# Performance work log

Hardware: AMD Instinct MI355X
Metric: run time of the kernel (lower is better)

The kernel has to match this reference:

```python
import math
import jax, jax.numpy as jnp
import numpy as np

NUM_HEADS = 16
NUM_LANDMARKS = 64


def setup_inputs() -> dict:
    key = jax.random.key(0)
    ks = jax.random.split(key, 14)
    B, S, H, M = 2, 4096, 1024, 512
    p = 0.02
    return {
        "hidden_states": jax.random.normal(ks[0], (B, S, H), jnp.float32),
        "Wq": jax.random.normal(ks[1], (H, H), jnp.float32) * p,
        "bq": jnp.zeros((H,), jnp.float32),
        "Wk": jax.random.normal(ks[2], (H, H), jnp.float32) * p,
        "bk": jnp.zeros((H,), jnp.float32),
        "Wv": jax.random.normal(ks[3], (H, H), jnp.float32) * p,
        "bv": jnp.zeros((H,), jnp.float32),
        "Wo": jax.random.normal(ks[4], (H, H), jnp.float32) * p,
        "bo": jnp.zeros((H,), jnp.float32),
        "mem_keys": jax.random.normal(ks[5], (M, H), jnp.float32) * p,
        "mem_values": jax.random.normal(ks[6], (M, H), jnp.float32) * p,
        "gate_w": jax.random.normal(ks[7], (H, 1), jnp.float32) * p,
        "gate_b": jnp.zeros((1,), jnp.float32),
        "top_k": 32,
    }


def reference(hidden_states, Wq, bq, Wk, bk, Wv, bv, Wo, bo,
              mem_keys, mem_values, gate_w, gate_b, top_k):
    B, S, H = hidden_states.shape
    nh, L = NUM_HEADS, NUM_LANDMARKS
    hd = H // nh

    # ---- landmark selection ('attention' method, no external attn weights) ----
    importance = jnp.linalg.norm(hidden_states, axis=-1)           # [B,S]
    _, lm_idx = jax.lax.top_k(importance, L)                       # [B,L]
    lm_idx = jnp.sort(lm_idx, axis=-1)
    landmark_hidden = jnp.take_along_axis(
        hidden_states, lm_idx[..., None], axis=1)                  # [B,L,H]

    # ---- landmark attention: all tokens attend to L landmarks ----
    q = (hidden_states @ Wq + bq).reshape(B, S, nh, hd)
    k = (landmark_hidden @ Wk + bk).reshape(B, L, nh, hd)
    v = (landmark_hidden @ Wv + bv).reshape(B, L, nh, hd)
    scores = jnp.einsum('bshd,blhd->bhsl', q, k) / math.sqrt(hd)   # [B,nh,S,L]
    attn = jax.nn.softmax(scores, axis=-1)
    ctx = jnp.einsum('bhsl,blhd->bshd', attn, v).reshape(B, S, H)
    landmark_out = ctx @ Wo + bo                                   # [B,S,H]

    # ---- memory bank read (top-k over M memory slots) ----
    mscores = jnp.einsum('bsh,mh->bsm', hidden_states, mem_keys) / math.sqrt(H)
    top_scores, top_idx = jax.lax.top_k(mscores, top_k)            # [B,S,K]
    top_vals = mem_values[top_idx]                                 # [B,S,K,H]
    mattn = jax.nn.softmax(top_scores, axis=-1)
    mem_out = jnp.einsum('bsk,bskh->bsh', mattn, top_vals)         # [B,S,H]
    gate = jax.nn.sigmoid(hidden_states @ gate_w + gate_b)         # [B,S,1]
    mem_out = gate * mem_out

    return landmark_out + mem_out
```

## Files before the change

kernel.cpp:

```cpp
#include <hip/hip_runtime.h>
#include <math.h>

#define HDIM 1024
#define NHEAD 16
#define HD 64
#define LM 64
#define MS 512
#define KSEL 32
#define NB 2
#define NS 4096
#define NTOK (NB*NS)

typedef __attribute__((ext_vector_type(8))) short short8;
typedef __attribute__((ext_vector_type(4))) float f32x4;
typedef __attribute__((ext_vector_type(4))) unsigned short us4;

__device__ __forceinline__ unsigned short f2bf(float f) {
  unsigned int u = __float_as_uint(f);
  unsigned int r = (u + 0x7fffu + ((u >> 16) & 1u)) >> 16;
  return (unsigned short)r;
}
__device__ __forceinline__ float bf2f(unsigned short u) {
  return __uint_as_float(((unsigned int)u) << 16);
}

__device__ __forceinline__ void gload_lds16(const unsigned short* g, unsigned short* l) {
  __builtin_amdgcn_global_load_lds(
      (const __attribute__((address_space(1))) unsigned int*)g,
      (__attribute__((address_space(3))) unsigned int*)l,
      16, 0, 0);
}

__global__ __launch_bounds__(256) void imp_gate_kernel(
    const float* __restrict__ hs, const float* __restrict__ gw,
    const float* __restrict__ gb, float* __restrict__ imp,
    float* __restrict__ gate, unsigned short* __restrict__ hsb) {
  const int lane = threadIdx.x & 63, wave = threadIdx.x >> 6;
  const int row = blockIdx.x*4 + wave;
  float ss = 0.f, dg = 0.f;
#pragma unroll
  for (int c = 0; c < 4; ++c) {
    const int d = c*256 + lane*4;
    const float4 hv = *(const float4*)(hs + (size_t)row*HDIM + d);
    const float4 gv = *(const float4*)(gw + d);
    ss += hv.x*hv.x + hv.y*hv.y + hv.z*hv.z + hv.w*hv.w;
    dg += hv.x*gv.x + hv.y*gv.y + hv.z*gv.z + hv.w*gv.w;
    us4 hb;
    hb.x = f2bf(hv.x); hb.y = f2bf(hv.y); hb.z = f2bf(hv.z); hb.w = f2bf(hv.w);
    *(us4*)(hsb + (size_t)row*HDIM + d) = hb;
  }
#pragma unroll
  for (int off = 32; off > 0; off >>= 1) {
    ss += __shfl_xor(ss, off);
    dg += __shfl_xor(dg, off);
  }
  if (lane == 0) {
    imp[row] = ss;
    gate[row] = 1.f/(1.f + expf(-(dg + gb[0])));
  }
}

__global__ __launch_bounds__(256) void lm_count_kernel(
    const float* __restrict__ imp, int* __restrict__ cnt) {
  const int b = blockIdx.z;
  const int jc = blockIdx.y;
  const int i = blockIdx.x*256 + threadIdx.x;
  const float* v = imp + b*NS;
  const float mine = v[i];
  __shared__ float tile[1024];
  const int j0 = jc*1024;
  *(float4*)&tile[threadIdx.x*4] = *(const float4*)&v[j0 + threadIdx.x*4];
  __syncthreads();
  int c = 0;
#pragma unroll 8
  for (int p = 0; p < 1024; p += 4) {
    const float4 t = *(const float4*)&tile[p];
    c += (t.x > mine) || (t.x == mine && (j0+p+0) < i);
    c += (t.y > mine) || (t.y == mine && (j0+p+1) < i);
    c += (t.z > mine) || (t.z == mine && (j0+p+2) < i);
    c += (t.w > mine) || (t.w == mine && (j0+p+3) < i);
  }
  atomicAdd(&cnt[b*NS + i], c);
}

__global__ __launch_bounds__(256) void lm_sel_kernel(
    const int* __restrict__ cnt, int* __restrict__ lm_idx) {
  const int b = blockIdx.y;
  const int i = blockIdx.x*256 + threadIdx.x;
  const int c = cnt[b*NS + i];
  if (c < LM) lm_idx[b*LM + c] = i;
}

__global__ __launch_bounds__(256) void lm_gather_kernel(
    const unsigned short* __restrict__ hsb, const int* __restrict__ lmi,
    unsigned short* __restrict__ g) {
  const int j = blockIdx.x;
  const int b = j >> 6;
  const int idx = lmi[j];
  const us4 v = *(const us4*)(hsb + ((size_t)(b*NS + idx))*HDIM + threadIdx.x*4);
  *(us4*)(g + (size_t)j*HDIM + threadIdx.x*4) = v;
}

__global__ __launch_bounds__(256) void kvproj_gemm_kernel(
    const unsigned short* __restrict__ g, const unsigned short* __restrict__ Wkvt,
    float* __restrict__ part) {
  __shared__ __align__(16) unsigned short As[128*32];
  __shared__ __align__(16) unsigned short Bs[128*32];
  const int tid = threadIdx.x;
  const int lane = tid & 63, wave = tid >> 6;
  const int wr = wave >> 1, wc = wave & 1;
  const int col0 = blockIdx.x << 7;
  const int sp = blockIdx.y;
  const int k00 = sp << 8;

  f32x4 acc[4][4];
#pragma unroll
  for (int m = 0; m < 4; ++m)
#pragma unroll
    for (int n = 0; n < 4; ++n) acc[m][n] = (f32x4)(0.f);

  const int srow = tid >> 2;
  const int sk   = (tid & 3) << 3;
  const unsigned short* gA = g    + (size_t)srow*HDIM + sk;
  const unsigned short* gB = Wkvt + (size_t)(col0 + srow)*HDIM + sk;
  const int fr = lane & 15;
  const int fk = (lane >> 4) << 3;
  const int fg = lane >> 4;

  for (int k0 = k00; k0 < k00 + 256; k0 += 32) {
    gload_lds16(gA + k0,             As + tid*8);
    gload_lds16(gA + 64*HDIM + k0,   As + 2048 + tid*8);
    gload_lds16(gB + k0,             Bs + tid*8);
    gload_lds16(gB + 64*HDIM + k0,   Bs + 2048 + tid*8);
    __syncthreads();
    short8 af[4], bf[4];
#pragma unroll
    for (int m = 0; m < 4; ++m)
      af[m] = *(const short8*)&As[(wr*64 + m*16 + fr)*32 + fk];
#pragma unroll
    for (int n = 0; n < 4; ++n)
      bf[n] = *(const short8*)&Bs[(wc*64 + n*16 + fr)*32 + fk];
#pragma unroll
    for (int m = 0; m < 4; ++m)
#pragma unroll
      for (int n = 0; n < 4; ++n)
        acc[m][n] = __builtin_amdgcn_mfma_f32_16x16x32_bf16(af[m], bf[n], acc[m][n], 0, 0, 0);
    __syncthreads();
  }
#pragma unroll
  for (int m = 0; m < 4; ++m)
#pragma unroll
    for (int n = 0; n < 4; ++n) {
      const int colg = col0 + wc*64 + n*16 + fr;
#pragma unroll
      for (int r = 0; r < 4; ++r) {
        const int row = wr*64 + m*16 + fg*4 + r;
        part[((size_t)(sp*128 + row))*2048 + colg] = acc[m][n][r];
      }
    }
}

__global__ __launch_bounds__(256) void kv_reduce2_kernel(
    const float* __restrict__ part, const float* __restrict__ bk,
    const float* __restrict__ bv, float* __restrict__ kbuf,
    float* __restrict__ vbuf) {
  const int row = blockIdx.y;
  const int col = blockIdx.x*256 + threadIdx.x;
  float s = 0.f;
#pragma unroll
  for (int sp = 0; sp < 4; ++sp)
    s += part[((size_t)(sp*128 + row))*2048 + col];
  if (col < HDIM) kbuf[(size_t)row*HDIM + col] = s + bk[col];
  else            vbuf[(size_t)row*HDIM + col - HDIM] = s + bv[col - HDIM];
}

__global__ __launch_bounds__(256) void prep_kernel(
    const float* __restrict__ Wk, const float* __restrict__ Wv,
    const float* __restrict__ Wq, const float* __restrict__ Wo,
    const float* __restrict__ mk, const float* __restrict__ mv,
    unsigned short* __restrict__ Wkvt, unsigned short* __restrict__ Wcat,
    unsigned short* __restrict__ Wot, unsigned short* __restrict__ mvT) {
  const int z = blockIdx.z;
  __shared__ float tile[32][33];
  const int tx = threadIdx.x & 31, ty = threadIdx.x >> 5;
  if (z < 4) {
    const float* W = (z == 0) ? Wk : (z == 1) ? Wv : (z == 2) ? Wq : Wo;
    unsigned short* Wt = (z == 0) ? Wkvt
                       : (z == 1) ? (Wkvt + (size_t)HDIM*HDIM)
                       : (z == 2) ? Wcat : Wot;
    const int bx = blockIdx.x * 32, by = blockIdx.y * 32;
#pragma unroll
    for (int i = 0; i < 32; i += 8)
      tile[ty + i][tx] = W[(size_t)(by + ty + i)*HDIM + bx + tx];
    __syncthreads();
#pragma unroll
    for (int i = 0; i < 32; i += 8)
      Wt[(size_t)(bx + ty + i)*HDIM + by + tx] = f2bf(tile[tx][ty + i]);
  } else {
    const int blk = blockIdx.y*32 + blockIdx.x;
    if (blk < 512) {
      const int off = (blk << 10) + threadIdx.x*4;
      const float4 v = *(const float4*)&mk[off];
      us4 w;
      w.x = f2bf(v.x); w.y = f2bf(v.y); w.z = f2bf(v.z); w.w = f2bf(v.w);
      *(us4*)&(Wcat + (size_t)HDIM*HDIM)[off] = w;
    } else {
      const int t = blk - 512;
      const int by = (t >> 5) * 32;
      const int bx = (t & 31) * 32;
#pragma unroll
      for (int i = 0; i < 32; i += 8)
        tile[ty + i][tx] = mv[(size_t)(by + ty + i)*HDIM + bx + tx];
      __syncthreads();
#pragma unroll
      for (int i = 0; i < 32; i += 8)
        mvT[(size_t)(bx + ty + i)*MS + by + tx] = f2bf(tile[tx][ty + i]);
    }
  }
}

__global__ __launch_bounds__(256) void gemm_qmsc_kernel(
    const unsigned short* __restrict__ A, const unsigned short* __restrict__ Bt,
    const float* __restrict__ bq, unsigned short* __restrict__ qb,
    float* __restrict__ msc) {
  __shared__ __align__(16) unsigned short As[128*32];
  __shared__ __align__(16) unsigned short Bs[128*32];
  const int tid = threadIdx.x;
  const int lane = tid & 63, wave = tid >> 6;
  const int wr = wave >> 1, wc = wave & 1;
  const int wg = blockIdx.x;
  const int swz = (wg & 7)*96 + (wg >> 3);
  const int bx = swz % 12, by = swz / 12;
  const int row0 = by << 7, col0 = bx << 7;

  f32x4 acc[4][4];
#pragma unroll
  for (int m = 0; m < 4; ++m)
#pragma unroll
    for (int n = 0; n < 4; ++n) acc[m][n] = (f32x4)(0.f);

  const int srow = tid >> 2;
  const int sk   = (tid & 3) << 3;
  const unsigned short* gA = A  + (size_t)(row0 + srow)*HDIM + sk;
  const unsigned short* gB = Bt + (size_t)(col0 + srow)*HDIM + sk;
  const int fr = lane & 15;
  const int fk = (lane >> 4) << 3;
  const int fg = lane >> 4;

  for (int k0 = 0; k0 < HDIM; k0 += 32) {
    gload_lds16(gA + k0,             As + tid*8);
    gload_lds16(gA + 64*HDIM + k0,   As + 2048 + tid*8);
    gload_lds16(gB + k0,             Bs + tid*8);
    gload_lds16(gB + 64*HDIM + k0,   Bs + 2048 + tid*8);
    __syncthreads();
    short8 af[4], bf[4];
#pragma unroll
    for (int m = 0; m < 4; ++m)
      af[m] = *(const short8*)&As[(wr*64 + m*16 + fr)*32 + fk];
#pragma unroll
    for (int n = 0; n < 4; ++n)
      bf[n] = *(const short8*)&Bs[(wc*64 + n*16 + fr)*32 + fk];
#pragma unroll
    for (int m = 0; m < 4; ++m)
#pragma unroll
      for (int n = 0; n < 4; ++n)
        acc[m][n] = __builtin_amdgcn_mfma_f32_16x16x32_bf16(af[m], bf[n], acc[m][n], 0, 0, 0);
    __syncthreads();
  }

#pragma unroll
  for (int m = 0; m < 4; ++m) {
#pragma unroll
    for (int n = 0; n < 4; ++n) {
      const int col = col0 + wc*64 + n*16 + fr;
      if (col < HDIM) {
        const float bb = bq[col];
#pragma unroll
        for (int r = 0; r < 4; ++r) {
          const int row = row0 + wr*64 + m*16 + fg*4 + r;
          qb[(size_t)row*HDIM + col] = f2bf(acc[m][n][r] + bb);
        }
      } else {
        const int c2 = col - HDIM;
#pragma unroll
        for (int r = 0; r < 4; ++r) {
          const int row = row0 + wr*64 + m*16 + fg*4 + r;
          msc[(size_t)row*MS + c2] = acc[m][n][r]*0.03125f;
        }
      }
    }
  }
}

__global__ __launch_bounds__(256) void attn_mfma_kernel(
    const unsigned short* __restrict__ qb, const float* __restrict__ kbuf,
    const float* __restrict__ vbuf, unsigned short* __restrict__ ctxb) {
  const int tb = blockIdx.x, h = blockIdx.y, b = blockIdx.z;
  const int tid = threadIdx.x;
  const int lane = tid & 63, wave = tid >> 6;
  __shared__ __align__(16) unsigned short Qs[128*64];
  __shared__ __align__(16) unsigned short Ks[64*64];
  __shared__ __align__(16) unsigned short Vt[64*64];
  __shared__ __align__(16) unsigned short Ps[128*64];

  const int tok0 = b*NS + tb*128;
#pragma unroll
  for (int it = 0; it < 4; ++it) {
    const int idx = it*256 + tid;
    gload_lds16(qb + (size_t)(tok0 + (idx >> 3))*HDIM + h*64 + (idx & 7)*8,
                Qs + idx*8);
  }
#pragma unroll
  for (int it = 0; it < 4; ++it) {
    const int i = it*256 + tid;
    const int l = i >> 4, d0 = (i & 15) << 2;
    const size_t base = (size_t)(b*LM + l)*HDIM + h*64 + d0;
    const float4 kv = *(const float4*)(kbuf + base);
    const float4 vv = *(const float4*)(vbuf + base);
    us4 k4; k4.x = f2bf(kv.x); k4.y = f2bf(kv.y); k4.z = f2bf(kv.z); k4.w = f2bf(kv.w);
    *(us4*)&Ks[l*64 + d0] = k4;
    Vt[(d0+0)*64 + l] = f2bf(vv.x);
    Vt[(d0+1)*64 + l] = f2bf(vv.y);
    Vt[(d0+2)*64 + l] = f2bf(vv.z);
    Vt[(d0+3)*64 + l] = f2bf(vv.w);
  }
  __syncthreads();

  const int fr = lane & 15;
  const int fg = lane >> 4;
  const int fk = fg << 3;
  const int wrow = wave*32;

  f32x4 acc[2][4];
#pragma unroll
  for (int m = 0; m < 2; ++m)
#pragma unroll
    for (int n = 0; n < 4; ++n) acc[m][n] = (f32x4)(0.f);
#pragma unroll
  for (int ks = 0; ks < 2; ++ks) {
    short8 af[2], bf[4];
#pragma unroll
    for (int m = 0; m < 2; ++m)
      af[m] = *(const short8*)&Qs[(wrow + m*16 + fr)*64 + ks*32 + fk];
#pragma unroll
    for (int n = 0; n < 4; ++n)
      bf[n] = *(const short8*)&Ks[(n*16 + fr)*64 + ks*32 + fk];
#pragma unroll
    for (int m = 0; m < 2; ++m)
#pragma unroll
      for (int n = 0; n < 4; ++n)
        acc[m][n] = __builtin_amdgcn_mfma_f32_16x16x32_bf16(af[m], bf[n], acc[m][n], 0, 0, 0);
  }

#pragma unroll
  for (int m = 0; m < 2; ++m) {
#pragma unroll
    for (int r = 0; r < 4; ++r) {
      float p0 = acc[m][0][r]*0.125f, p1 = acc[m][1][r]*0.125f;
      float p2 = acc[m][2][r]*0.125f, p3 = acc[m][3][r]*0.125f;
      float mx = fmaxf(fmaxf(p0, p1), fmaxf(p2, p3));
#pragma unroll
      for (int off = 1; off < 16; off <<= 1) mx = fmaxf(mx, __shfl_xor(mx, off));
      p0 = expf(p0 - mx); p1 = expf(p1 - mx); p2 = expf(p2 - mx); p3 = expf(p3 - mx);
      float sm = p0 + p1 + p2 + p3;
#pragma unroll
      for (int off = 1; off < 16; off <<= 1) sm += __shfl_xor(sm, off);
      const float inv = 1.f/sm;
      const int prow = (wrow + m*16 + fg*4 + r)*64;
      Ps[prow + 0*16 + fr] = f2bf(p0*inv);
      Ps[prow + 1*16 + fr] = f2bf(p1*inv);
      Ps[prow + 2*16 + fr] = f2bf(p2*inv);
      Ps[prow + 3*16 + fr] = f2bf(p3*inv);
    }
  }
  __syncthreads();

  f32x4 occ[2][4];
#pragma unroll
  for (int m = 0; m < 2; ++m)
#pragma unroll
    for (int n = 0; n < 4; ++n) occ[m][n] = (f32x4)(0.f);
#pragma unroll
  for (int ks = 0; ks < 2; ++ks) {
    short8 af[2], bf[4];
#pragma unroll
    for (int m = 0; m < 2; ++m)
      af[m] = *(const short8*)&Ps[(wrow + m*16 + fr)*64 + ks*32 + fk];
#pragma unroll
    for (int n = 0; n < 4; ++n)
      bf[n] = *(const short8*)&Vt[(n*16 + fr)*64 + ks*32 + fk];
#pragma unroll
    for (int m = 0; m < 2; ++m)
#pragma unroll
      for (int n = 0; n < 4; ++n)
        occ[m][n] = __builtin_amdgcn_mfma_f32_16x16x32_bf16(af[m], bf[n], occ[m][n], 0, 0, 0);
  }
#pragma unroll
  for (int m = 0; m < 2; ++m)
#pragma unroll
    for (int n = 0; n < 4; ++n)
#pragma unroll
      for (int r = 0; r < 4; ++r)
        ctxb[(size_t)(tok0 + wrow + m*16 + fg*4 + r)*HDIM + h*64 + n*16 + fr] =
            f2bf(occ[m][n][r]);
}

__global__ __launch_bounds__(256) void sel_kernel(
    const float* __restrict__ msc, const float* __restrict__ gate,
    unsigned short* __restrict__ Wm) {
  const int tid = threadIdx.x;
  const int lane = tid & 63, wave = tid >> 6;
  const int token = blockIdx.x*4 + wave;

  __shared__ __align__(16) int s_hist[4][256];
  __shared__ unsigned long long s_list[4][256];
  __shared__ int s_B[4], s_above[4], s_nlist[4];

  *(int4*)&s_hist[wave][lane*4] = make_int4(0, 0, 0, 0);
  if (lane == 0) s_nlist[wave] = 0;

  float v[8];
#pragma unroll
  for (int j = 0; j < 8; ++j) v[j] = msc[(size_t)token*MS + j*64 + lane];

  float mx = v[0], mn = v[0];
#pragma unroll
  for (int j = 1; j < 8; ++j) { mx = fmaxf(mx, v[j]); mn = fminf(mn, v[j]); }
#pragma unroll
  for (int off = 32; off > 0; off >>= 1) {
    mx = fmaxf(mx, __shfl_xor(mx, off));
    mn = fminf(mn, __shfl_xor(mn, off));
  }
  const float range = mx - mn;
  const float scale = (range > 1e-20f) ? 255.f/range : 0.f;

  __builtin_amdgcn_wave_barrier();
  int bins[8];
#pragma unroll
  for (int j = 0; j < 8; ++j) {
    int b = (int)((v[j] - mn)*scale);
    bins[j] = b > 255 ? 255 : b;
    atomicAdd(&s_hist[wave][bins[j]], 1);
  }
  __builtin_amdgcn_wave_barrier();

  const int4 c = *(const int4*)&s_hist[wave][lane*4];
  const int lane_total = c.x + c.y + c.z + c.w;
  int sfx = lane_total;
#pragma unroll
  for (int off = 1; off < 64; off <<= 1) {
    const int src = lane + off;
    int y = __shfl(sfx, src < 64 ? src : lane);
    sfx += (src < 64) ? y : 0;
  }
  const int beyond = sfx - lane_total;
  const int s3 = c.w + beyond;
  const int s2 = c.z + s3;
  const int s1 = c.y + s2;
  const int s0 = c.x + s1;
  int Bl = -1, abv = 0;
  if (s0 >= KSEL && s1 < KSEL) { Bl = lane*4 + 0; abv = s1; }
  if (s1 >= KSEL && s2 < KSEL) { Bl = lane*4 + 1; abv = s2; }
  if (s2 >= KSEL && s3 < KSEL) { Bl = lane*4 + 2; abv = s3; }
  if (s3 >= KSEL && beyond < KSEL) { Bl = lane*4 + 3; abv = beyond; }
  if (Bl >= 0) { s_B[wave] = Bl; s_above[wave] = abv; }
  __builtin_amdgcn_wave_barrier();
  const int B = s_B[wave];
  const int rem = KSEL - s_above[wave];

#pragma unroll
  for (int j = 0; j < 8; ++j) {
    if (bins[j] == B) {
      const unsigned int u = __float_as_uint(v[j]);
      const unsigned int vk = (u & 0x80000000u) ? ~u : (u | 0x80000000u);
      const int p = atomicAdd(&s_nlist[wave], 1);
      if (p < 256)
        s_list[wave][p] = ((unsigned long long)vk << 32) | (unsigned int)~(j*64 + lane);
    }
  }
  __builtin_amdgcn_wave_barrier();

  const int nl = s_nlist[wave] < 256 ? s_nlist[wave] : 256;
  unsigned long long T = ~0ull;
  for (int r = 0; r < rem; ++r) {
    unsigned long long best = 0; int pos = -1;
    for (int i = lane; i < nl; i += 64)
      if (s_list[wave][i] > best) { best = s_list[wave][i]; pos = i; }
#pragma unroll
    for (int off = 32; off > 0; off >>= 1) {
      const unsigned long long ob = __shfl_xor(best, off);
      const int op = __shfl_xor(pos, off);
      if (ob > best) { best = ob; pos = op; }
    }
    if (lane == 0) s_list[wave][pos] = 0;
    T = best;
    __builtin_amdgcn_wave_barrier();
  }

  float e[8];
  float esum = 0.f;
#pragma unroll
  for (int j = 0; j < 8; ++j) {
    bool sel = bins[j] > B;
    if (!sel && bins[j] == B) {
      const unsigned int u = __float_as_uint(v[j]);
      const unsigned int vk = (u & 0x80000000u) ? ~u : (u | 0x80000000u);
      const unsigned long long key =
          ((unsigned long long)vk << 32) | (unsigned int)~(j*64 + lane);
      sel = key >= T;
    }
    e[j] = sel ? expf(v[j] - mx) : 0.f;
    esum += e[j];
  }
#pragma unroll
  for (int off = 32; off > 0; off >>= 1) esum += __shfl_xor(esum, off);
  const float ginv = gate[token]/esum;
#pragma unroll
  for (int j = 0; j < 8; ++j)
    Wm[(size_t)token*MS + j*64 + lane] = f2bf(e[j]*ginv);
}

__global__ __launch_bounds__(256) void gemm_fused_out_kernel(
    const unsigned short* __restrict__ A,
    const unsigned short* __restrict__ Bt,
    const unsigned short* __restrict__ Wm,
    const unsigned short* __restrict__ mvT,
    const float* __restrict__ bias, float* __restrict__ out) {
  __shared__ __align__(16) unsigned short As[128*32];
  __shared__ __align__(16) unsigned short Bs[128*32];
  const int tid = threadIdx.x;
  const int lane = tid & 63, wave = tid >> 6;
  const int wr = wave >> 1, wc = wave & 1;
  const int wg = blockIdx.x;
  const int swz = (wg & 7)*64 + (wg >> 3);
  const int bx = swz & 7, by = swz >> 3;
  const int row0 = by << 7, col0 = bx << 7;

  f32x4 acc[4][4];
#pragma unroll
  for (int m = 0; m < 4; ++m)
#pragma unroll
    for (int n = 0; n < 4; ++n) acc[m][n] = (f32x4)(0.f);

  const int srow = tid >> 2;
  const int sk   = (tid & 3) << 3;
  const int fr = lane & 15;
  const int fk = (lane >> 4) << 3;
  const int fg = lane >> 4;

  {
    const unsigned short* gA = A  + (size_t)(row0 + srow)*HDIM + sk;
    const unsigned short* gB = Bt + (size_t)(col0 + srow)*HDIM + sk;
    for (int k0 = 0; k0 < HDIM; k0 += 32) {
      gload_lds16(gA + k0,             As + tid*8);
      gload_lds16(gA + 64*HDIM + k0,   As + 2048 + tid*8);
      gload_lds16(gB + k0,             Bs + tid*8);
      gload_lds16(gB + 64*HDIM + k0,   Bs + 2048 + tid*8);
      __syncthreads();
      short8 af[4], bf[4];
#pragma unroll
      for (int m = 0; m < 4; ++m)
        af[m] = *(const short8*)&As[(wr*64 + m*16 + fr)*32 + fk];
#pragma unroll
      for (int n = 0; n < 4; ++n)
        bf[n] = *(const short8*)&Bs[(wc*64 + n*16 + fr)*32 + fk];
#pragma unroll
      for (int m = 0; m < 4; ++m)
#pragma unroll
        for (int n = 0; n < 4; ++n)
          acc[m][n] = __builtin_amdgcn_mfma_f32_16x16x32_bf16(af[m], bf[n], acc[m][n], 0, 0, 0);
      __syncthreads();
    }
  }
  {
    const unsigned short* gA = Wm  + (size_t)(row0 + srow)*MS + sk;
    const unsigned short* gB = mvT + (size_t)(col0 + srow)*MS + sk;
    for (int k0 = 0; k0 < MS; k0 += 32) {
      gload_lds16(gA + k0,           As + tid*8);
      gload_lds16(gA + 64*MS + k0,   As + 2048 + tid*8);
      gload_lds16(gB + k0,           Bs + tid*8);
      gload_lds16(gB + 64*MS + k0,   Bs + 2048 + tid*8);
      __syncthreads();
      short8 af[4], bf[4];
#pragma unroll
      for (int m = 0; m < 4; ++m)
        af[m] = *(const short8*)&As[(wr*64 + m*16 + fr)*32 + fk];
#pragma unroll
      for (int n = 0; n < 4; ++n)
        bf[n] = *(const short8*)&Bs[(wc*64 + n*16 + fr)*32 + fk];
#pragma unroll
      for (int m = 0; m < 4; ++m)
#pragma unroll
        for (int n = 0; n < 4; ++n)
          acc[m][n] = __builtin_amdgcn_mfma_f32_16x16x32_bf16(af[m], bf[n], acc[m][n], 0, 0, 0);
      __syncthreads();
    }
  }

#pragma unroll
  for (int m = 0; m < 4; ++m) {
#pragma unroll
    for (int n = 0; n < 4; ++n) {
      const int col = col0 + wc*64 + n*16 + fr;
      const float bb = bias[col];
#pragma unroll
      for (int r = 0; r < 4; ++r) {
        const int row = row0 + wr*64 + m*16 + fg*4 + r;
        out[(size_t)row*HDIM + col] = acc[m][n][r] + bb;
      }
    }
  }
}

extern "C" void kernel_launch(void* const* d_in, const int* in_sizes, int n_in,
                              void* d_out, int out_size, void* d_ws, size_t ws_size,
                              hipStream_t stream) {
  const float* hs = (const float*)d_in[0];
  const float* Wq = (const float*)d_in[1];
  const float* bq = (const float*)d_in[2];
  const float* Wk = (const float*)d_in[3];
  const float* bk = (const float*)d_in[4];
  const float* Wv = (const float*)d_in[5];
  const float* bv = (const float*)d_in[6];
  const float* Wo = (const float*)d_in[7];
  const float* bo = (const float*)d_in[8];
  const float* mk = (const float*)d_in[9];
  const float* mv = (const float*)d_in[10];
  const float* gw = (const float*)d_in[11];
  const float* gb = (const float*)d_in[12];
  float* out = (float*)d_out;

  char* ws = (char*)d_ws;
  unsigned short* hsb  = (unsigned short*)(ws);
  unsigned short* ctxb = hsb;
  unsigned short* qb   = (unsigned short*)(ws + ((size_t)16 << 20));
  unsigned short* Wm   = qb;
  float*          msc  = (float*)(ws + ((size_t)32 << 20));
  unsigned short* Wkvt = (unsigned short*)(ws + ((size_t)48 << 20));
  unsigned short* Wcat = (unsigned short*)(ws + ((size_t)52 << 20));
  unsigned short* Wot  = (unsigned short*)(ws + ((size_t)55 << 20));
  unsigned short* mvT  = (unsigned short*)(ws + ((size_t)57 << 20));
  float*          kbuf = (float*)(ws + ((size_t)58 << 20));
  float*          vbuf = (float*)(ws + ((size_t)58 << 20) + ((size_t)512 << 10));
  unsigned short* g    = (unsigned short*)(ws + ((size_t)59 << 20));
  float*          part = (float*)(ws + ((size_t)59 << 20) + ((size_t)256 << 10));
  float*          imp  = (float*)(ws + ((size_t)64 << 20));
  float*          gate = (float*)(ws + ((size_t)64 << 20) + ((size_t)32 << 10));
  int*            cnt  = (int*)  (ws + ((size_t)64 << 20) + ((size_t)64 << 10));
  int*            lmi  = (int*)  (ws + ((size_t)64 << 20) + ((size_t)96 << 10));

  imp_gate_kernel<<<dim3(NTOK/4), 256, 0, stream>>>(hs, gw, gb, imp, gate, hsb);
  hipMemsetAsync(cnt, 0, NB*NS*sizeof(int), stream);
  lm_count_kernel<<<dim3(NS/256, 4, NB), 256, 0, stream>>>(imp, cnt);
  lm_sel_kernel<<<dim3(NS/256, NB), 256, 0, stream>>>(cnt, lmi);
  prep_kernel<<<dim3(32, 32, 5), 256, 0, stream>>>(
      Wk, Wv, Wq, Wo, mk, mv, Wkvt, Wcat, Wot, mvT);
  lm_gather_kernel<<<dim3(NB*LM), 256, 0, stream>>>(hsb, lmi, g);
  kvproj_gemm_kernel<<<dim3(16, 4), 256, 0, stream>>>(g, Wkvt, part);
  kv_reduce2_kernel<<<dim3(8, 128), 256, 0, stream>>>(part, bk, bv, kbuf, vbuf);
  gemm_qmsc_kernel<<<dim3(768), 256, 0, stream>>>(hsb, Wcat, bq, qb, msc);
  attn_mfma_kernel<<<dim3(NS/128, NHEAD, NB), 256, 0, stream>>>(qb, kbuf, vbuf, ctxb);
  sel_kernel<<<dim3(NTOK/4), 256, 0, stream>>>(msc, gate, Wm);
  gemm_fused_out_kernel<<<dim3(512), 256, 0, stream>>>(ctxb, Wot, Wm, mvT, bo, out);
}
```

Before: 167.9 us.

## Use 64-wide XOR-swizzled K tiles in GEMMs and reuse Q LDS for P

Both bf16 MFMA GEMM kernels now stage 64-wide K slices per iteration instead of 32. Each thread loads four 16-byte chunks, and chunk positions are XOR-swizzled by row so the short8 fragment reads avoid LDS bank conflicts. This halves the number of barrier pairs per GEMM and doubles LDS use per block, which may lower occupancy. In the attention kernel the softmax probabilities are written into the Q shared buffer instead of a separate P buffer, and the barrier before the PV product is dropped. That relies on each wave reading back only its own rows.

Result: faster. 163.6 us (-2.5%).

```diff
diff --git a/kernel.cpp b/kernel.cpp
--- a/kernel.cpp
+++ b/kernel.cpp
@@ -30,6 +30,15 @@
       (__attribute__((address_space(3))) unsigned int*)l,
       16, 0, 0);
 }
+
+#define STAGE64(gbase, k0, LDA, lds)                                          \
+  {                                                                           \
+    const unsigned short* _s = (gbase) + (k0) + gchk*8;                       \
+    gload_lds16(_s,                 (lds) + tid*8);                           \
+    gload_lds16(_s + (size_t)32*(LDA), (lds) + 2048 + tid*8);                 \
+    gload_lds16(_s + (size_t)64*(LDA), (lds) + 4096 + tid*8);                 \
+    gload_lds16(_s + (size_t)96*(LDA), (lds) + 6144 + tid*8);                 \
+  }
 
 __global__ __launch_bounds__(256) void imp_gate_kernel(
     const float* __restrict__ hs, const float* __restrict__ gw,
@@ -223,8 +232,8 @@
     const unsigned short* __restrict__ A, const unsigned short* __restrict__ Bt,
     const float* __restrict__ bq, unsigned short* __restrict__ qb,
     float* __restrict__ msc) {
-  __shared__ __align__(16) unsigned short As[128*32];
-  __shared__ __align__(16) unsigned short Bs[128*32];
+  __shared__ __align__(16) unsigned short As[128*64];
+  __shared__ __align__(16) unsigned short Bs[128*64];
   const int tid = threadIdx.x;
   const int lane = tid & 63, wave = tid >> 6;
   const int wr = wave >> 1, wc = wave & 1;
@@ -239,32 +248,35 @@
 #pragma unroll
     for (int n = 0; n < 4; ++n) acc[m][n] = (f32x4)(0.f);
 
-  const int srow = tid >> 2;
-  const int sk   = (tid & 3) << 3;
-  const unsigned short* gA = A  + (size_t)(row0 + srow)*HDIM + sk;
-  const unsigned short* gB = Bt + (size_t)(col0 + srow)*HDIM + sk;
+  const int srow = tid >> 3;
+  const int gchk = (tid & 7) ^ (srow & 7);
+  const unsigned short* gA = A  + (size_t)(row0 + srow)*HDIM;
+  const unsigned short* gB = Bt + (size_t)(col0 + srow)*HDIM;
   const int fr = lane & 15;
-  const int fk = (lane >> 4) << 3;
   const int fg = lane >> 4;
-
-  for (int k0 = 0; k0 < HDIM; k0 += 32) {
-    gload_lds16(gA + k0,             As + tid*8);
-    gload_lds16(gA + 64*HDIM + k0,   As + 2048 + tid*8);
-    gload_lds16(gB + k0,             Bs + tid*8);
-    gload_lds16(gB + 64*HDIM + k0,   Bs + 2048 + tid*8);
+  const int ca = ((0*4 + fg) ^ (fr & 7)) * 8;
+  const int cb = ((1*4 + fg) ^ (fr & 7)) * 8;
+
+  for (int k0 = 0; k0 < HDIM; k0 += 64) {
+    STAGE64(gA, k0, HDIM, As);
+    STAGE64(gB, k0, HDIM, Bs);
     __syncthreads();
-    short8 af[4], bf[4];
-#pragma unroll
-    for (int m = 0; m < 4; ++m)
-      af[m] = *(const short8*)&As[(wr*64 + m*16 + fr)*32 + fk];
-#pragma unroll
-    for (int n = 0; n < 4; ++n)
-      bf[n] = *(const short8*)&Bs[(wc*64 + n*16 + fr)*32 + fk];
-#pragma unroll
-    for (int m = 0; m < 4; ++m)
+#pragma unroll
+    for (int kh = 0; kh < 2; ++kh) {
+      const int cc = kh ? cb : ca;
+      short8 af[4], bf[4];
+#pragma unroll
+      for (int m = 0; m < 4; ++m)
+        af[m] = *(const short8*)&As[(wr*64 + m*16 + fr)*64 + cc];
 #pragma unroll
       for (int n = 0; n < 4; ++n)
-        acc[m][n] = __builtin_amdgcn_mfma_f32_16x16x32_bf16(af[m], bf[n], acc[m][n], 0, 0, 0);
+        bf[n] = *(const short8*)&Bs[(wc*64 + n*16 + fr)*64 + cc];
+#pragma unroll
+      for (int m = 0; m < 4; ++m)
+#pragma unroll
+        for (int n = 0; n < 4; ++n)
+          acc[m][n] = __builtin_amdgcn_mfma_f32_16x16x32_bf16(af[m], bf[n], acc[m][n], 0, 0, 0);
+    }
     __syncthreads();
   }
 
@@ -301,7 +313,6 @@
   __shared__ __align__(16) unsigned short Qs[128*64];
   __shared__ __align__(16) unsigned short Ks[64*64];
   __shared__ __align__(16) unsigned short Vt[64*64];
-  __shared__ __align__(16) unsigned short Ps[128*64];
 
   const int tok0 = b*NS + tb*128;
 #pragma unroll
@@ -367,13 +378,12 @@
       for (int off = 1; off < 16; off <<= 1) sm += __shfl_xor(sm, off);
       const float inv = 1.f/sm;
       const int prow = (wrow + m*16 + fg*4 + r)*64;
-      Ps[prow + 0*16 + fr] = f2bf(p0*inv);
-      Ps[prow + 1*16 + fr] = f2bf(p1*inv);
-      Ps[prow + 2*16 + fr] = f2bf(p2*inv);
-      Ps[prow + 3*16 + fr] = f2bf(p3*inv);
-    }
-  }
-  __syncthreads();
+      Qs[prow + 0*16 + fr] = f2bf(p0*inv);
+      Qs[prow + 1*16 + fr] = f2bf(p1*inv);
+      Qs[prow + 2*16 + fr] = f2bf(p2*inv);
+      Qs[prow + 3*16 + fr] = f2bf(p3*inv);
+    }
+  }
 
   f32x4 occ[2][4];
 #pragma unroll
@@ -385,7 +395,7 @@
     short8 af[2], bf[4];
 #pragma unroll
     for (int m = 0; m < 2; ++m)
-      af[m] = *(const short8*)&Ps[(wrow + m*16 + fr)*64 + ks*32 + fk];
+      af[m] = *(const short8*)&Qs[(wrow + m*16 + fr)*64 + ks*32 + fk];
 #pragma unroll
     for (int n = 0; n < 4; ++n)
       bf[n] = *(const short8*)&Vt[(n*16 + fr)*64 + ks*32 + fk];
@@ -526,8 +536,8 @@
     const unsigned short* __restrict__ Wm,
     const unsigned short* __restrict__ mvT,
     const float* __restrict__ bias, float* __restrict__ out) {
-  __shared__ __align__(16) unsigned short As[128*32];
-  __shared__ __align__(16) unsigned short Bs[128*32];
+  __shared__ __align__(16) unsigned short As[128*64];
+  __shared__ __align__(16) unsigned short Bs[128*64];
   const int tid = threadIdx.x;
   const int lane = tid & 63, wave = tid >> 6;
   const int wr = wave >> 1, wc = wave & 1;
@@ -542,57 +552,62 @@
 #pragma unroll
     for (int n = 0; n < 4; ++n) acc[m][n] = (f32x4)(0.f);
 
-  const int srow = tid >> 2;
-  const int sk   = (tid & 3) << 3;
+  const int srow = tid >> 3;
+  const int gchk = (tid & 7) ^ (srow & 7);
   const int fr = lane & 15;
-  const int fk = (lane >> 4) << 3;
   const int fg = lane >> 4;
+  const int ca = ((0*4 + fg) ^ (fr & 7)) * 8;
+  const int cb = ((1*4 + fg) ^ (fr & 7)) * 8;
 
   {
-    const unsigned short* gA = A  + (size_t)(row0 + srow)*HDIM + sk;
-    const unsigned short* gB = Bt + (size_t)(col0 + srow)*HDIM + sk;
-    for (int k0 = 0; k0 < HDIM; k0 += 32) {
-      gload_lds16(gA + k0,             As + tid*8);
-      gload_lds16(gA + 64*HDIM + k0,   As + 2048 + tid*8);
-      gload_lds16(gB + k0,             Bs + tid*8);
-      gload_lds16(gB + 64*HDIM + k0,   Bs + 2048 + tid*8);
+    const unsigned short* gA = A  + (size_t)(row0 + srow)*HDIM;
+    const unsigned short* gB = Bt + (size_t)(col0 + srow)*HDIM;
+    for (int k0 = 0; k0 < HDIM; k0 += 64) {
+      STAGE64(gA, k0, HDIM, As);
+      STAGE64(gB, k0, HDIM, Bs);
       __syncthreads();
-      short8 af[4], bf[4];
-#pragma unroll
-      for (int m = 0; m < 4; ++m)
-        af[m] = *(const short8*)&As[(wr*64 + m*16 + fr)*32 + fk];
-#pragma unroll
-      for (int n = 0; n < 4; ++n)
-        bf[n] = *(const short8*)&Bs[(wc*64 + n*16 + fr)*32 + fk];
-#pragma unroll
-      for (int m = 0; m < 4; ++m)
+#pragma unroll
+      for (int kh = 0; kh < 2; ++kh) {
+        const int cc = kh ? cb : ca;
+        short8 af[4], bf[4];
+#pragma unroll
+        for (int m = 0; m < 4; ++m)
+          af[m] = *(const short8*)&As[(wr*64 + m*16 + fr)*64 + cc];
 #pragma unroll
         for (int n = 0; n < 4; ++n)
-          acc[m][n] = __builtin_amdgcn_mfma_f32_16x16x32_bf16(af[m], bf[n], acc[m][n], 0, 0, 0);
+          bf[n] = *(const short8*)&Bs[(wc*64 + n*16 + fr)*64 + cc];
+#pragma unroll
+        for (int m = 0; m < 4; ++m)
+#pragma unroll
+          for (int n = 0; n < 4; ++n)
+            acc[m][n] = __builtin_amdgcn_mfma_f32_16x16x32_bf16(af[m], bf[n], acc[m][n], 0, 0, 0);
+      }
       __syncthreads();
     }
   }
   {
-    const unsigned short* gA = Wm  + (size_t)(row0 + srow)*MS + sk;
-    const unsigned short* gB = mvT + (size_t)(col0 + srow)*MS + sk;
-    for (int k0 = 0; k0 < MS; k0 += 32) {
-      gload_lds16(gA + k0,           As + tid*8);
-      gload_lds16(gA + 64*MS + k0,   As + 2048 + tid*8);
-      gload_lds16(gB + k0,           Bs + tid*8);
-      gload_lds16(gB + 64*MS + k0,   Bs + 2048 + tid*8);
+    const unsigned short* gA = Wm  + (size_t)(row0 + srow)*MS;
+    const unsigned short* gB = mvT + (size_t)(col0 + srow)*MS;
+    for (int k0 = 0; k0 < MS; k0 += 64) {
+      STAGE64(gA, k0, MS, As);
+      STAGE64(gB, k0, MS, Bs);
       __syncthreads();
-      short8 af[4], bf[4];
-#pragma unroll
-      for (int m = 0; m < 4; ++m)
-        af[m] = *(const short8*)&As[(wr*64 + m*16 + fr)*32 + fk];
-#pragma unroll
-      for (int n = 0; n < 4; ++n)
-        bf[n] = *(const short8*)&Bs[(wc*64 + n*16 + fr)*32 + fk];
-#pragma unroll
-      for (int m = 0; m < 4; ++m)
+#pragma unroll
+      for (int kh = 0; kh < 2; ++kh) {
+        const int cc = kh ? cb : ca;
+        short8 af[4], bf[4];
+#pragma unroll
+        for (int m = 0; m < 4; ++m)
+          af[m] = *(const short8*)&As[(wr*64 + m*16 + fr)*64 + cc];
 #pragma unroll
         for (int n = 0; n < 4; ++n)
-          acc[m][n] = __builtin_amdgcn_mfma_f32_16x16x32_bf16(af[m], bf[n], acc[m][n], 0, 0, 0);
+          bf[n] = *(const short8*)&Bs[(wc*64 + n*16 + fr)*64 + cc];
+#pragma unroll
+        for (int m = 0; m < 4; ++m)
+#pragma unroll
+          for (int n = 0; n < 4; ++n)
+            acc[m][n] = __builtin_amdgcn_mfma_f32_16x16x32_bf16(af[m], bf[n], acc[m][n], 0, 0, 0);
+      }
       __syncthreads();
     }
   }
```
